# Kernel optimization log

Hardware: AMD Instinct MI355X
Metric: run time of the kernel (lower is better)

## Reference

```python
import jax, jax.numpy as jnp
import numpy as np

LATDIM = 128
ANCHOR_SET_NUM = 64
N_NODES = 10000

def setup_inputs() -> dict:
    key = jax.random.key(0)
    k1, k2, k3, k4, k5 = jax.random.split(key, 5)
    embeds = jax.random.normal(k1, (N_NODES, LATDIM), dtype=jnp.float32)
    dists_array = jax.random.uniform(k2, (ANCHOR_SET_NUM, N_NODES), dtype=jnp.float32)
    W_hidden = jax.random.normal(k3, (LATDIM, 2 * LATDIM), dtype=jnp.float32) * 0.05
    b_hidden = jax.random.normal(k4, (LATDIM,), dtype=jnp.float32) * 0.05
    anchorset_id = jax.random.randint(k5, (ANCHOR_SET_NUM,), 0, N_NODES, dtype=jnp.int64 if jax.config.jax_enable_x64 else jnp.int32)
    return {"embeds": embeds, "dists_array": dists_array, "W_hidden": W_hidden,
            "b_hidden": b_hidden, "anchorset_id": anchorset_id}

def reference(embeds, dists_array, W_hidden, b_hidden, anchorset_id):
    A, N = dists_array.shape
    d = embeds.shape[1]
    set_ids_emb = embeds[anchorset_id]                       # [A, d] anchor gather
    # messages[i, j] = set_ids_emb[j] * dists[j, i]
    messages = set_ids_emb[None, :, :] * dists_array.T[:, :, None]   # [N, A, d]
    # faithful to torch: embeds.repeat(A,1).reshape(-1, A, d) -> embeds[(i*A+j) % N]
    self_feature = jnp.tile(embeds, (A, 1)).reshape(N, A, d)          # [N, A, d]
    m = jnp.concatenate([messages, self_feature], axis=-1)            # [N, A, 2d]
    h = jnp.einsum('nak,ok->nao', m, W_hidden) + b_hidden             # [N, A, d]
    return jnp.mean(h, axis=1)                                        # [N, d]
```

## Files before the change

### kernel.cpp

```cpp
#include <hip/hip_runtime.h>

#define LATDIM 128
#define ANUM   64
#define NNODES 10000
#define PERIOD 625
#define NJ     16


__global__ __launch_bounds__(256) void fused_kernel(
    const float* __restrict__ embeds,
    const float* __restrict__ dists,
    const float* __restrict__ W,
    const float* __restrict__ b,
    const int*   __restrict__ anchor,
    float* __restrict__ out)
{
    __shared__ float EA[ANUM * LATDIM];
    __shared__ float G_s[NJ * LATDIM];
    __shared__ float D_s[ANUM * NJ];
    __shared__ float S_s[LATDIM];
    __shared__ int   An[ANUM];

    const int tid = threadIdx.x;
    const int orig = blockIdx.x;
    const int xcd = orig & 7, ii = orig >> 3;
    const int s = (xcd == 0) ? ii : (79 + (xcd - 1) * 78 + ii);

    if (tid < ANUM) An[tid] = anchor[tid];
    #pragma unroll
    for (int it = 0; it < 4; ++it) {
        int idx = it * 256 + tid;
        int a = idx >> 4, j = idx & 15;
        D_s[a * NJ + j] = dists[(size_t)a * NNODES + (s + PERIOD * j)];
    }
    float (*Xp)[LATDIM] = (float (*)[LATDIM])G_s;
    {
        const int row0 = (64 * s) % NNODES;
        const int c4 = tid & 31, hg = tid >> 5;
        float4 sum = {0.f, 0.f, 0.f, 0.f};
        #pragma unroll
        for (int i = 0; i < 8; ++i) {
            int row = row0 + 8 * i + hg;
            if (row >= NNODES) row -= NNODES;
            float4 v = *((const float4*)(embeds + (size_t)row * LATDIM) + c4);
            sum.x += v.x; sum.y += v.y; sum.z += v.z; sum.w += v.w;
        }
        ((float4*)&Xp[hg][0])[c4] = sum;
    }
    __syncthreads();

    if (tid < LATDIM) {
        float t = Xp[0][tid];
        #pragma unroll
        for (int g = 1; g < 8; ++g) t += Xp[g][tid];
        S_s[tid] = t;
    }
    #pragma unroll
    for (int it = 0; it < 8; ++it) {
        int idx = it * 256 + tid;
        int a = idx >> 5, c4 = idx & 31;
        ((float4*)EA)[a * 32 + c4] =
            *((const float4*)(embeds + (size_t)An[a] * LATDIM) + c4);
    }
    __syncthreads();

    {
        const int k  = tid & 127;
        const int jh = tid >> 7;
        float g[8] = {};
        #pragma unroll
        for (int a = 0; a < ANUM; ++a) {
            const float  ea = EA[a * LATDIM + k];
            const float4 d0 = ((const float4*)(D_s + a * NJ + jh * 8))[0];
            const float4 d1 = ((const float4*)(D_s + a * NJ + jh * 8))[1];
            g[0] += d0.x * ea; g[1] += d0.y * ea;
            g[2] += d0.z * ea; g[3] += d0.w * ea;
            g[4] += d1.x * ea; g[5] += d1.y * ea;
            g[6] += d1.z * ea; g[7] += d1.w * ea;
        }
        #pragma unroll
        for (int jj = 0; jj < 8; ++jj)
            G_s[(jh * 8 + jj) * LATDIM + k] = g[jj];
    }
    __syncthreads();

    {
        const int o = tid & 127;
        const int h = tid >> 7;
        const float4* Wr1 = (const float4*)(W + (size_t)o * (2 * LATDIM) + h * 64);
        const float4* Wr2 = (const float4*)(W + (size_t)o * (2 * LATDIM) + LATDIM + h * 64);
        const float4* S4  = (const float4*)S_s;
        const float4* G4  = (const float4*)G_s;
        float acc[NJ] = {};
        float sacc = 0.f;
        #pragma unroll
        for (int q = 0; q < 16; ++q) {
            const float4 w1 = Wr1[q];
            const float4 w2 = Wr2[q];
            const float4 sv = S4[h * 16 + q];
            sacc += sv.x*w2.x + sv.y*w2.y + sv.z*w2.z + sv.w*w2.w;
            #pragma unroll
            for (int j = 0; j < NJ; ++j) {
                const float4 gv = G4[j * 32 + h * 16 + q];
                acc[j] += gv.x*w1.x + gv.y*w1.y + gv.z*w1.z + gv.w*w1.w;
            }
        }
        float* R = EA;
        if (h == 1) {
            #pragma unroll
            for (int j = 0; j < NJ; ++j)
                R[j * LATDIM + o] = acc[j] + sacc;
        }
        __syncthreads();
        if (h == 0) {
            const float bias = b[o];
            #pragma unroll
            for (int j = 0; j < NJ; ++j) {
                const int n = s + PERIOD * j;
                out[(size_t)n * LATDIM + o] =
                    bias + (acc[j] + sacc + R[j * LATDIM + o]) * (1.0f / ANUM);
            }
        }
    }
}

extern "C" void kernel_launch(void* const* d_in, const int* in_sizes, int n_in,
                              void* d_out, int out_size, void* d_ws, size_t ws_size,
                              hipStream_t stream) {
    const float* embeds = (const float*)d_in[0];
    const float* dists  = (const float*)d_in[1];
    const float* W      = (const float*)d_in[2];
    const float* b      = (const float*)d_in[3];
    const int*   anchor = (const int*)d_in[4];
    float* out = (float*)d_out;

    (void)d_ws; (void)ws_size;
    fused_kernel<<<PERIOD, 256, 0, stream>>>(embeds, dists, W, b, anchor, out);
}
```

Measured before the change: 88.13 us.

## Drop anchor smem tile, read anchors from global, and split GEMV with lane shuffles

Removes the 32KB anchor-embedding shared buffer and reads anchor rows straight from global/L2 inside the gather loop, cutting LDS use so more blocks fit per CU (launch bounds now request 6). The output projection is restructured: adjacent lanes split the K dimension and combine their partial sums with a shuffle, and each thread handles two outputs over 8 node slots. This replaces the shared-memory reduction and its barrier. The cost is repeated global loads of anchor rows and register pressure from the occupancy hint.

```diff
diff --git a/kernel.cpp b/kernel.cpp
--- a/kernel.cpp
+++ b/kernel.cpp
@@ -7,7 +7,7 @@
 #define NJ     16
 
 
-__global__ __launch_bounds__(256) void fused_kernel(
+__global__ __launch_bounds__(256, 6) void fused_kernel(
     const float* __restrict__ embeds,
     const float* __restrict__ dists,
     const float* __restrict__ W,
@@ -15,7 +15,6 @@
     const int*   __restrict__ anchor,
     float* __restrict__ out)
 {
-    __shared__ float EA[ANUM * LATDIM];
     __shared__ float G_s[NJ * LATDIM];
     __shared__ float D_s[ANUM * NJ];
     __shared__ float S_s[LATDIM];
@@ -55,22 +54,14 @@
         for (int g = 1; g < 8; ++g) t += Xp[g][tid];
         S_s[tid] = t;
     }
-    #pragma unroll
-    for (int it = 0; it < 8; ++it) {
-        int idx = it * 256 + tid;
-        int a = idx >> 5, c4 = idx & 31;
-        ((float4*)EA)[a * 32 + c4] =
-            *((const float4*)(embeds + (size_t)An[a] * LATDIM) + c4);
-    }
-    __syncthreads();
 
     {
         const int k  = tid & 127;
         const int jh = tid >> 7;
         float g[8] = {};
-        #pragma unroll
+        #pragma unroll 8
         for (int a = 0; a < ANUM; ++a) {
-            const float  ea = EA[a * LATDIM + k];
+            const float ea = embeds[(size_t)An[a] * LATDIM + k];
             const float4 d0 = ((const float4*)(D_s + a * NJ + jh * 8))[0];
             const float4 d1 = ((const float4*)(D_s + a * NJ + jh * 8))[1];
             g[0] += d0.x * ea; g[1] += d0.y * ea;
@@ -78,6 +69,7 @@
             g[4] += d1.x * ea; g[5] += d1.y * ea;
             g[6] += d1.z * ea; g[7] += d1.w * ea;
         }
+        __syncthreads();
         #pragma unroll
         for (int jj = 0; jj < 8; ++jj)
             G_s[(jh * 8 + jj) * LATDIM + k] = g[jj];
@@ -85,41 +77,46 @@
     __syncthreads();
 
     {
-        const int o = tid & 127;
-        const int h = tid >> 7;
-        const float4* Wr1 = (const float4*)(W + (size_t)o * (2 * LATDIM) + h * 64);
-        const float4* Wr2 = (const float4*)(W + (size_t)o * (2 * LATDIM) + LATDIM + h * 64);
+        const int o  = tid & 127;
+        const int h  = tid & 1;
+        const int jg = tid >> 7;
+        const float4* Wf4 = (const float4*)W;
+        const float4* w1p = Wf4 + (size_t)(o & ~1) * 64 + h * 16;
+        const float4* w2p = w1p + 32;
+        const float4* G4  = (const float4*)G_s;
         const float4* S4  = (const float4*)S_s;
-        const float4* G4  = (const float4*)G_s;
-        float acc[NJ] = {};
-        float sacc = 0.f;
-        #pragma unroll
+
+        float acc[16] = {};
+        float sacc0 = 0.f, sacc1 = 0.f;
+        #pragma unroll 4
         for (int q = 0; q < 16; ++q) {
-            const float4 w1 = Wr1[q];
-            const float4 w2 = Wr2[q];
+            const float4 wa = w1p[q];
+            const float4 wb = w1p[64 + q];
+            const float4 va = w2p[q];
+            const float4 vb = w2p[64 + q];
             const float4 sv = S4[h * 16 + q];
-            sacc += sv.x*w2.x + sv.y*w2.y + sv.z*w2.z + sv.w*w2.w;
+            sacc0 += sv.x*va.x + sv.y*va.y + sv.z*va.z + sv.w*va.w;
+            sacc1 += sv.x*vb.x + sv.y*vb.y + sv.z*vb.z + sv.w*vb.w;
             #pragma unroll
-            for (int j = 0; j < NJ; ++j) {
-                const float4 gv = G4[j * 32 + h * 16 + q];
-                acc[j] += gv.x*w1.x + gv.y*w1.y + gv.z*w1.z + gv.w*w1.w;
+            for (int jj = 0; jj < 8; ++jj) {
+                const float4 gv = G4[(jg * 8 + jj) * 32 + h * 16 + q];
+                acc[jj*2+0] += gv.x*wa.x + gv.y*wa.y + gv.z*wa.z + gv.w*wa.w;
+                acc[jj*2+1] += gv.x*wb.x + gv.y*wb.y + gv.z*wb.z + gv.w*wb.w;
             }
         }
-        float* R = EA;
-        if (h == 1) {
-            #pragma unroll
-            for (int j = 0; j < NJ; ++j)
-                R[j * LATDIM + o] = acc[j] + sacc;
-        }
-        __syncthreads();
-        if (h == 0) {
-            const float bias = b[o];
-            #pragma unroll
-            for (int j = 0; j < NJ; ++j) {
-                const int n = s + PERIOD * j;
-                out[(size_t)n * LATDIM + o] =
-                    bias + (acc[j] + sacc + R[j * LATDIM + o]) * (1.0f / ANUM);
-            }
+
+        const float bias = b[o];
+        float s_mine = h ? sacc1 : sacc0;
+        float s_src  = h ? sacc0 : sacc1;
+        float s_full = s_mine + __shfl_xor(s_src, 1);
+        #pragma unroll
+        for (int jj = 0; jj < 8; ++jj) {
+            float m  = h ? acc[jj*2+1] : acc[jj*2+0];
+            float xs = h ? acc[jj*2+0] : acc[jj*2+1];
+            float gfull = m + __shfl_xor(xs, 1);
+            const int n = s + PERIOD * (jg * 8 + jj);
+            out[(size_t)n * LATDIM + o] =
+                bias + (gfull + s_full) * (1.0f / ANUM);
         }
     }
 }
```

Measured after the change: 108.0 us. +22.5%, slower.

## Split each residue class across two blocks and drop anchor staging in LDS

Applied to the files above, without the earlier changes.

Doubles the grid to 1250 blocks so that each block handles 8 of the 16 output rows sharing a residue, with a new XCD-aware block-to-work mapping. The 32KB shared anchor-embedding tile is removed and anchor rows are read straight from global/L2 inside the anchor loop. The aim is more blocks and lower LDS use per block, giving higher occupancy and better coverage of the CUs. In exchange, the self-feature row sum and the anchor reads are now repeated by both blocks of each pair.

```diff
diff --git a/kernel.cpp b/kernel.cpp
--- a/kernel.cpp
+++ b/kernel.cpp
@@ -4,7 +4,8 @@
 #define ANUM   64
 #define NNODES 10000
 #define PERIOD 625
-#define NJ     16
+#define JB     8
+#define NB     1250
 
 
 __global__ __launch_bounds__(256) void fused_kernel(
@@ -15,23 +16,27 @@
     const int*   __restrict__ anchor,
     float* __restrict__ out)
 {
-    __shared__ float EA[ANUM * LATDIM];
-    __shared__ float G_s[NJ * LATDIM];
-    __shared__ float D_s[ANUM * NJ];
+    __shared__ float G_s[JB * LATDIM];
+    __shared__ float R_s[JB * LATDIM];
+    __shared__ float D_s[ANUM * JB];
     __shared__ float S_s[LATDIM];
     __shared__ int   An[ANUM];
 
     const int tid = threadIdx.x;
     const int orig = blockIdx.x;
     const int xcd = orig & 7, ii = orig >> 3;
-    const int s = (xcd == 0) ? ii : (79 + (xcd - 1) * 78 + ii);
+    const int u = (xcd < 2) ? (xcd * 157 + ii)
+                            : (2 * 157 + (xcd - 2) * 156 + ii);
+    const int s = u >> 1;
+    const int jhalf = u & 1;
 
     if (tid < ANUM) An[tid] = anchor[tid];
     #pragma unroll
-    for (int it = 0; it < 4; ++it) {
+    for (int it = 0; it < 2; ++it) {
         int idx = it * 256 + tid;
-        int a = idx >> 4, j = idx & 15;
-        D_s[a * NJ + j] = dists[(size_t)a * NNODES + (s + PERIOD * j)];
+        int a = idx >> 3, j8 = idx & 7;
+        D_s[a * JB + j8] =
+            dists[(size_t)a * NNODES + (s + PERIOD * (jhalf * JB + j8))];
     }
     float (*Xp)[LATDIM] = (float (*)[LATDIM])G_s;
     {
@@ -55,32 +60,22 @@
         for (int g = 1; g < 8; ++g) t += Xp[g][tid];
         S_s[tid] = t;
     }
-    #pragma unroll
-    for (int it = 0; it < 8; ++it) {
-        int idx = it * 256 + tid;
-        int a = idx >> 5, c4 = idx & 31;
-        ((float4*)EA)[a * 32 + c4] =
-            *((const float4*)(embeds + (size_t)An[a] * LATDIM) + c4);
-    }
-    __syncthreads();
 
     {
         const int k  = tid & 127;
-        const int jh = tid >> 7;
-        float g[8] = {};
+        const int jq = tid >> 7;
+        float g[4] = {};
+        #pragma unroll 8
+        for (int a = 0; a < ANUM; ++a) {
+            const float ea = embeds[(size_t)An[a] * LATDIM + k];
+            const float4 d = ((const float4*)(D_s + a * JB))[jq];
+            g[0] += d.x * ea; g[1] += d.y * ea;
+            g[2] += d.z * ea; g[3] += d.w * ea;
+        }
+        __syncthreads();
         #pragma unroll
-        for (int a = 0; a < ANUM; ++a) {
-            const float  ea = EA[a * LATDIM + k];
-            const float4 d0 = ((const float4*)(D_s + a * NJ + jh * 8))[0];
-            const float4 d1 = ((const float4*)(D_s + a * NJ + jh * 8))[1];
-            g[0] += d0.x * ea; g[1] += d0.y * ea;
-            g[2] += d0.z * ea; g[3] += d0.w * ea;
-            g[4] += d1.x * ea; g[5] += d1.y * ea;
-            g[6] += d1.z * ea; g[7] += d1.w * ea;
-        }
-        #pragma unroll
-        for (int jj = 0; jj < 8; ++jj)
-            G_s[(jh * 8 + jj) * LATDIM + k] = g[jj];
+        for (int jj = 0; jj < 4; ++jj)
+            G_s[(jq * 4 + jj) * LATDIM + k] = g[jj];
     }
     __syncthreads();
 
@@ -88,37 +83,36 @@
         const int o = tid & 127;
         const int h = tid >> 7;
         const float4* Wr1 = (const float4*)(W + (size_t)o * (2 * LATDIM) + h * 64);
-        const float4* Wr2 = (const float4*)(W + (size_t)o * (2 * LATDIM) + LATDIM + h * 64);
+        const float4* Wr2 = Wr1 + 32;
         const float4* S4  = (const float4*)S_s;
         const float4* G4  = (const float4*)G_s;
-        float acc[NJ] = {};
+        float acc[JB] = {};
         float sacc = 0.f;
-        #pragma unroll
+        #pragma unroll 4
         for (int q = 0; q < 16; ++q) {
             const float4 w1 = Wr1[q];
             const float4 w2 = Wr2[q];
             const float4 sv = S4[h * 16 + q];
             sacc += sv.x*w2.x + sv.y*w2.y + sv.z*w2.z + sv.w*w2.w;
             #pragma unroll
-            for (int j = 0; j < NJ; ++j) {
+            for (int j = 0; j < JB; ++j) {
                 const float4 gv = G4[j * 32 + h * 16 + q];
                 acc[j] += gv.x*w1.x + gv.y*w1.y + gv.z*w1.z + gv.w*w1.w;
             }
         }
-        float* R = EA;
         if (h == 1) {
             #pragma unroll
-            for (int j = 0; j < NJ; ++j)
-                R[j * LATDIM + o] = acc[j] + sacc;
+            for (int j = 0; j < JB; ++j)
+                R_s[j * LATDIM + o] = acc[j] + sacc;
         }
         __syncthreads();
         if (h == 0) {
             const float bias = b[o];
             #pragma unroll
-            for (int j = 0; j < NJ; ++j) {
-                const int n = s + PERIOD * j;
+            for (int j = 0; j < JB; ++j) {
+                const int n = s + PERIOD * (jhalf * JB + j);
                 out[(size_t)n * LATDIM + o] =
-                    bias + (acc[j] + sacc + R[j * LATDIM + o]) * (1.0f / ANUM);
+                    bias + (acc[j] + sacc + R_s[j * LATDIM + o]) * (1.0f / ANUM);
             }
         }
     }
@@ -135,5 +129,5 @@
     float* out = (float*)d_out;
 
     (void)d_ws; (void)ws_size;
-    fused_kernel<<<PERIOD, 256, 0, stream>>>(embeds, dists, W, b, anchor, out);
+    fused_kernel<<<NB, 256, 0, stream>>>(embeds, dists, W, b, anchor, out);
 }
```

After: 94.59 us. 7.3% more time.
